# Kernel tuning notes

Hardware: AMD Instinct MI355X
Metric: run time of the kernel (lower is better)

## Reference

```python
import jax, jax.numpy as jnp
import numpy as np

M, U, H, C, EMB, HID = 4096, 8, 8, 64, 64, 128
N = M * U            # 32768 nodes
E = 131072           # edges
D = H * C            # 512 = heads * hidden_channels
NUM_LAYERS = 4
IN0 = 6              # 2 coords + mask + speed + cost + arrival
SCALE = np.float32(1.0 / np.sqrt(C))

def _lin(x, W, b):
    return x @ W + b

def _transformer_conv(x, src, dst, Wq, bq, Wk, bk, Wv, bv, Ws, bs):
    # PyG TransformerConv: x_j = x[src], x_i = x[dst]; softmax over edges per dst
    n = x.shape[0]
    q = _lin(x, Wq, bq).reshape(n, H, C)
    k = _lin(x, Wk, bk).reshape(n, H, C)
    v = _lin(x, Wv, bv).reshape(n, H, C)
    alpha = jnp.einsum('ehc,ehc->eh', q[dst], k[src]) * SCALE   # [E,H]
    amax = jax.ops.segment_max(alpha, dst, num_segments=n)       # [N,H]
    ex = jnp.exp(alpha - amax[dst])
    denom = jax.ops.segment_sum(ex, dst, num_segments=n)         # [N,H]
    agg = jax.ops.segment_sum(ex[:, :, None] * v[src], dst, num_segments=n)  # [N,H,C]
    out = agg / (denom[:, :, None] + 1e-16)
    return out.reshape(n, D) + _lin(x, Ws, bs)                   # concat heads + root skip

def _forward(mission_coords, uavs_info, speeds, cost_matrix, arrival_times,
             Wq0, bq0, Wk0, bk0, Wv0, bv0, Ws0, bs0,
             Wq, bq, Wk, bk, Wv, bv, Ws, bs,
             fc_W, fc_b, aW1, ab1, aW2, ab2, cW1, cb1, cW2, cb2,
             edge_index, batch, action_mask):
    mc = jnp.broadcast_to(mission_coords[:, None, :], (M, U, 2))
    mk = jnp.broadcast_to(action_mask[:, None, None].astype(jnp.float32), (M, U, 1))
    sp = jnp.broadcast_to(speeds[None, :, None], (M, U, 1))
    cm = cost_matrix.T[:, :, None]
    at = arrival_times.T[:, :, None]
    x = jnp.concatenate([mc, mk, sp, cm, at], axis=-1).reshape(N, IN0)
    src, dst = edge_index[0], edge_index[1]
    x = jax.nn.relu(_transformer_conv(x, src, dst, Wq0, bq0, Wk0, bk0, Wv0, bv0, Ws0, bs0))
    for l in range(NUM_LAYERS - 1):
        x = jax.nn.relu(_transformer_conv(x, src, dst, Wq[l], bq[l], Wk[l], bk[l], Wv[l], bv[l], Ws[l], bs[l]))
    new_batch = jnp.repeat(batch, U)                             # [N]
    sums = jax.ops.segment_sum(x, new_batch, num_segments=1)
    cnts = jax.ops.segment_sum(jnp.ones((N,), x.dtype), new_batch, num_segments=1)
    pooled = sums / cnts[:, None]                                # [1, D]
    emb = _lin(pooled, fc_W, fc_b)                               # [1, EMB]
    emb_exp = jnp.tile(emb, (U, 1))                              # [U, EMB]
    combined = jnp.concatenate([uavs_info, emb_exp, speeds[:, None]], axis=-1)  # [U, EMB+3]
    action_probs = jax.nn.softmax(_lin(jax.nn.relu(_lin(combined, aW1, ab1)), aW2, ab2), axis=-1)
    state_values = _lin(jax.nn.relu(_lin(combined, cW1, cb1)), cW2, cb2)
    return action_probs, state_values

def setup_inputs() -> dict:
    key = jax.random.key(0)
    ks = jax.random.split(key, 40)
    def nrm(i, shape, s=0.05):
        return jax.random.normal(ks[i], shape, jnp.float32) * s
    z = lambda *s: jnp.zeros(s, jnp.float32)
    L = NUM_LAYERS - 1
    inp = dict(
        mission_coords=jax.random.uniform(ks[0], (M, 2), jnp.float32),
        uavs_info=nrm(1, (U, 2), 1.0),
        speeds=jax.random.uniform(ks[2], (U,), jnp.float32) + 0.5,
        cost_matrix=jax.random.uniform(ks[3], (U, M), jnp.float32),
        arrival_times=jax.random.uniform(ks[4], (U, M), jnp.float32),
        edge_index=jax.random.randint(ks[5], (2, E), 0, N),
        batch=jnp.zeros((M,), jnp.int32),
        action_mask=jax.random.randint(ks[6], (M,), 0, 2),
        Wq0=nrm(7, (IN0, D)), bq0=z(D), Wk0=nrm(8, (IN0, D)), bk0=z(D),
        Wv0=nrm(9, (IN0, D)), bv0=z(D), Ws0=nrm(10, (IN0, D)), bs0=z(D),
        Wq=nrm(11, (L, D, D)), bq=z(L, D), Wk=nrm(12, (L, D, D)), bk=z(L, D),
        Wv=nrm(13, (L, D, D)), bv=z(L, D), Ws=nrm(14, (L, D, D)), bs=z(L, D),
        fc_W=nrm(15, (D, EMB)), fc_b=z(EMB),
        aW1=nrm(16, (EMB + 3, HID)), ab1=z(HID), aW2=nrm(17, (HID, M)), ab2=z(M),
        cW1=nrm(18, (EMB + 3, HID)), cb1=z(HID), cW2=nrm(19, (HID, 1)), cb2=z(1),
    )
    return inp

def reference(mission_coords, edge_index, batch, uavs_info, action_mask, speeds,
              cost_matrix, arrival_times,
              Wq0, bq0, Wk0, bk0, Wv0, bv0, Ws0, bs0,
              Wq, bq, Wk, bk, Wv, bv, Ws, bs,
              fc_W, fc_b, aW1, ab1, aW2, ab2, cW1, cb1, cW2, cb2):
    return _forward(mission_coords, uavs_info, speeds, cost_matrix, arrival_times,
                    Wq0, bq0, Wk0, bk0, Wv0, bv0, Ws0, bs0,
                    Wq, bq, Wk, bk, Wv, bv, Ws, bs,
                    fc_W, fc_b, aW1, ab1, aW2, ab2, cW1, cb1, cW2, cb2,
                    edge_index, batch, action_mask)
```

## Files before the change

kernel.cpp:

```cpp
#include <hip/hip_runtime.h>
#include <stdint.h>

typedef unsigned short u16;
typedef __attribute__((ext_vector_type(8))) unsigned short u16x8;
typedef __attribute__((ext_vector_type(8))) __bf16 bf16x8;
typedef __attribute__((ext_vector_type(4))) float f32x4;
typedef __attribute__((ext_vector_type(2))) float f32x2;

#define NNODES 32768
#define NEDGES 131072
#define DDIM 512
#define QK4 2048
#define MM 4096
#define UU 8

__device__ __forceinline__ u16 f2bf(float f) {
    unsigned u = __builtin_bit_cast(unsigned, f);
    u += 0x7FFFu + ((u >> 16) & 1u);
    return (u16)(u >> 16);
}
__device__ __forceinline__ float bf2f(u16 h) {
    return __builtin_bit_cast(float, (unsigned)h << 16);
}

__device__ __forceinline__ void enc8(const float* f, int* lo, int* hi) {
    int a = __builtin_amdgcn_cvt_pk_fp8_f32(f[0], f[1], 0, false);
    a = __builtin_amdgcn_cvt_pk_fp8_f32(f[2], f[3], a, true);
    int b = __builtin_amdgcn_cvt_pk_fp8_f32(f[4], f[5], 0, false);
    b = __builtin_amdgcn_cvt_pk_fp8_f32(f[6], f[7], b, true);
    *lo = a;
    *hi = b;
}

__device__ __forceinline__ void load_lds16(const void* g, void* l) {
    __builtin_amdgcn_global_load_lds((__attribute__((address_space(1))) unsigned int*)(void*)g,
                                     (__attribute__((address_space(3))) unsigned int*)l, 16, 0, 0);
}

__global__ void k_zero(unsigned int* p, int n) {
    int i = blockIdx.x * 256 + threadIdx.x;
    if (i < n) p[i] = 0u;
}

__global__ void k_build_x0(const float* __restrict__ mc, const int* __restrict__ mask,
                           const float* __restrict__ sp, const float* __restrict__ cm,
                           const float* __restrict__ at, float* __restrict__ x0) {
    int node = blockIdx.x * 256 + threadIdx.x;
    if (node >= NNODES) return;
    int m = node >> 3, u = node & 7;
    float* o = x0 + (size_t)node * 6;
    o[0] = mc[m * 2];
    o[1] = mc[m * 2 + 1];
    o[2] = (float)mask[m];
    o[3] = sp[u];
    o[4] = cm[u * MM + m];
    o[5] = at[u * MM + m];
}

__global__ void k_w0cat(const float* __restrict__ Wq0, const float* __restrict__ Wk0,
                        const float* __restrict__ Wv0, const float* __restrict__ Ws0,
                        float* __restrict__ W0cat) {
    int i = blockIdx.x * 256 + threadIdx.x;
    if (i >= 6 * QK4) return;
    int k = i / QK4, n = i % QK4;
    int t = n >> 9, nn = n & 511;
    const float* p = (t == 0) ? Wq0 : (t == 1) ? Wk0 : (t == 2) ? Wv0 : Ws0;
    W0cat[i] = p[k * DDIM + nn];
}

__global__ void k_bcat(const float* __restrict__ bq0, const float* __restrict__ bk0,
                       const float* __restrict__ bv0, const float* __restrict__ bs0,
                       const float* __restrict__ bq, const float* __restrict__ bk,
                       const float* __restrict__ bv, const float* __restrict__ bs,
                       float* __restrict__ b0cat, float* __restrict__ bcat) {
    int i = blockIdx.x * 256 + threadIdx.x;
    if (i >= 4 * QK4) return;
    int n = i & (QK4 - 1);
    int l = i >> 11;
    int t = n >> 9, nn = n & 511;
    if (l == 0) {
        const float* p = (t == 0) ? bq0 : (t == 1) ? bk0 : (t == 2) ? bv0 : bs0;
        b0cat[n] = p[nn];
    } else {
        const float* p = (t == 0) ? bq : (t == 1) ? bk : (t == 2) ? bv : bs;
        bcat[(size_t)(l - 1) * QK4 + n] = p[(l - 1) * DDIM + nn];
    }
}

__global__ void k_wt(const float* __restrict__ Wq, const float* __restrict__ Wk,
                     const float* __restrict__ Wv, const float* __restrict__ Ws,
                     u16* __restrict__ Wt) {
    __shared__ float tile[32][33];
    int q = blockIdx.z;
    int l = q >> 2, t = q & 3;
    const float* src = ((t == 0) ? Wq : (t == 1) ? Wk : (t == 2) ? Wv : Ws) + (size_t)l * DDIM * DDIM;
    int k0 = blockIdx.x * 32, n0 = blockIdx.y * 32;
    int tx = threadIdx.x, ty = threadIdx.y;
#pragma unroll
    for (int r = 0; r < 4; r++) tile[ty + 8 * r][tx] = src[(size_t)(k0 + ty + 8 * r) * DDIM + n0 + tx];
    __syncthreads();
    u16* dst = Wt + (size_t)l * QK4 * DDIM + (size_t)t * DDIM * DDIM;
#pragma unroll
    for (int r = 0; r < 4; r++) {
        int n = n0 + ty + 8 * r;
        dst[(size_t)n * DDIM + k0 + tx] = f2bf(tile[tx][ty + 8 * r]);
    }
}

__global__ void k_count(const int* __restrict__ dst, int* __restrict__ deg) {
    int e = blockIdx.x * 256 + threadIdx.x;
    if (e < NEDGES) atomicAdd(&deg[dst[e]], 1);
}

__global__ __launch_bounds__(1024) void k_scan(const int* __restrict__ deg, int* __restrict__ offs,
                                               int* __restrict__ cursor) {
    __shared__ int sums[1024];
    int t = threadIdx.x;
    int base = t * 32;
    int local[32];
    int s = 0;
#pragma unroll
    for (int i = 0; i < 32; i++) { local[i] = s; s += deg[base + i]; }
    sums[t] = s;
    __syncthreads();
    for (int d = 1; d < 1024; d <<= 1) {
        int v = (t >= d) ? sums[t - d] : 0;
        __syncthreads();
        sums[t] += v;
        __syncthreads();
    }
    int excl = (t == 0) ? 0 : sums[t - 1];
#pragma unroll
    for (int i = 0; i < 32; i++) {
        int o = excl + local[i];
        offs[base + i] = o;
        cursor[base + i] = o;
    }
    if (t == 1023) offs[NNODES] = sums[1023];
}

__global__ void k_scatter(const int* __restrict__ src, const int* __restrict__ dst,
                          int* __restrict__ cursor, int* __restrict__ ssrc) {
    int e = blockIdx.x * 256 + threadIdx.x;
    if (e < NEDGES) {
        int pos = atomicAdd(&cursor[dst[e]], 1);
        ssrc[pos] = src[e];
    }
}

__global__ __launch_bounds__(256) void k_gemm0(const float* __restrict__ x0, const float* __restrict__ W0cat,
                                               const float* __restrict__ b0cat, u16* __restrict__ QS,
                                               unsigned char* __restrict__ KV8) {
    int node = blockIdx.x;
    int t = threadIdx.x;
    float xv[6];
#pragma unroll
    for (int k = 0; k < 6; k++) xv[k] = x0[(size_t)node * 6 + k];
    int n0 = t * 8;
    float f[8];
#pragma unroll
    for (int j = 0; j < 8; j++) {
        int n = n0 + j;
        float s = b0cat[n];
#pragma unroll
        for (int k = 0; k < 6; k++) s += xv[k] * W0cat[k * QK4 + n];
        f[j] = s;
    }
    if (n0 < 512) {
        u16x8 o;
#pragma unroll
        for (int j = 0; j < 8; j++) o[j] = f2bf(f[j]);
        *(u16x8*)(QS + (size_t)node * 1024 + n0) = o;
    } else if (n0 < 1536) {
        int lo, hi;
        enc8(f, &lo, &hi);
        int kvcol = (n0 < 1024) ? (n0 - 512) : (n0 - 1024);
        int ofs = (n0 < 1024) ? 0 : 8;
        *(int2*)(KV8 + (size_t)node * 1024 + (size_t)(kvcol >> 3) * 16 + ofs) = make_int2(lo, hi);
    } else {
        u16x8 o;
#pragma unroll
        for (int j = 0; j < 8; j++) o[j] = f2bf(f[j]);
        *(u16x8*)(QS + (size_t)node * 1024 + 512 + (n0 - 1536)) = o;
    }
}

__global__ __launch_bounds__(256, 4) void k_gemm(const u16* __restrict__ X, const u16* __restrict__ Wt,
                                                 const float* __restrict__ bcat, u16* __restrict__ QS,
                                                 unsigned char* __restrict__ KV8) {
    __shared__ __align__(16) u16 smem[2 * 128 * 64];
    u16* As = smem;
    u16* Bs = smem + 128 * 64;
    const int tid = threadIdx.x;
    const int lane = tid & 63;
    const int w = tid >> 6;
    const int wm = w & 1, wn = w >> 1;
    const int bid = blockIdx.x;
    const int xcd = bid & 7;
    const int s = bid >> 3;
    const size_t arow0 = (size_t)(xcd * 32 + (s >> 4)) * 128;
    const size_t brow0 = (size_t)(s & 15) * 128;
    const int bt = (int)(brow0 >> 7);

    f32x4 acc[4][4];
#pragma unroll
    for (int i = 0; i < 4; i++)
#pragma unroll
        for (int j = 0; j < 4; j++) acc[i][j] = (f32x4){0.f, 0.f, 0.f, 0.f};

    const int la = lane & 7;
    const int quad = lane >> 4;
    const int lm = lane & 15;

    for (int kt = 0; kt < 8; ++kt) {
        const int k0 = kt * 64;
#pragma unroll
        for (int t = 0; t < 4; ++t) {
            int idx = (w * 4 + t) * 64 + lane;
            int m = idx >> 3;
            int c = la ^ (m & 7);
            const u16* ga = X + (arow0 + m) * DDIM + (k0 + c * 8);
            const u16* gb = Wt + (brow0 + m) * DDIM + (k0 + c * 8);
            load_lds16(ga, &As[(size_t)((w * 4 + t) * 64) * 8]);
            load_lds16(gb, &Bs[(size_t)((w * 4 + t) * 64) * 8]);
        }
        __syncthreads();
#pragma unroll
        for (int kk = 0; kk < 2; ++kk) {
            bf16x8 af[4], bfg[4];
            int c = kk * 4 + quad;
#pragma unroll
            for (int i = 0; i < 4; ++i) {
                int m = wm * 64 + i * 16 + lm;
                int slot = m * 8 + (c ^ (m & 7));
                af[i] = *(const bf16x8*)&As[(size_t)slot * 8];
            }
#pragma unroll
            for (int j = 0; j < 4; ++j) {
                int n = wn * 64 + j * 16 + lm;
                int slot = n * 8 + (c ^ (n & 7));
                bfg[j] = *(const bf16x8*)&Bs[(size_t)slot * 8];
            }
#pragma unroll
            for (int i = 0; i < 4; ++i)
#pragma unroll
                for (int j = 0; j < 4; ++j)
                    acc[i][j] = __builtin_amdgcn_mfma_f32_16x16x32_bf16(af[i], bfg[j], acc[i][j], 0, 0, 0);
        }
        __syncthreads();
    }

    float biasv[4];
#pragma unroll
    for (int j = 0; j < 4; ++j) biasv[j] = bcat[brow0 + wn * 64 + j * 16 + lm];

    u16* stg = smem;
    const int chunk = lane & 7;
    const int rrow = lane >> 3;
    const int colbase = (int)brow0 + wn * 64 + chunk * 8;
#pragma unroll
    for (int p = 0; p < 2; ++p) {
        __syncthreads();
#pragma unroll
        for (int ii = 0; ii < 2; ++ii) {
            int i = p * 2 + ii;
#pragma unroll
            for (int j = 0; j < 4; ++j) {
#pragma unroll
                for (int r = 0; r < 4; ++r) {
                    int lr = ii * 16 + quad * 4 + r;
                    int lc = j * 16 + lm;
                    stg[(size_t)(w * 32 + lr) * 72 + lc] = f2bf(acc[i][j][r] + biasv[j]);
                }
            }
        }
        __syncthreads();
#pragma unroll
        for (int it = 0; it < 4; ++it) {
            int row = it * 8 + rrow;
            u16x8 v = *(const u16x8*)&stg[(size_t)(w * 32 + row) * 72 + chunk * 8];
            size_t grow = arow0 + wm * 64 + p * 32 + row;
            if (bt < 4) {
                *(u16x8*)&QS[grow * 1024 + colbase] = v;
            } else if (bt < 12) {
                float f[8];
#pragma unroll
                for (int j = 0; j < 8; j++) f[j] = bf2f(v[j]);
                int lo, hi;
                enc8(f, &lo, &hi);
                int kvcol = (bt < 8) ? (colbase - 512) : (colbase - 1024);
                int ofs = (bt < 8) ? 0 : 8;
                *(int2*)(KV8 + grow * 1024 + (size_t)(kvcol >> 3) * 16 + ofs) = make_int2(lo, hi);
            } else {
                *(u16x8*)&QS[grow * 1024 + 512 + (colbase - 1536)] = v;
            }
        }
    }
}

__global__ __launch_bounds__(256) void k_attn(const u16* __restrict__ QS, const unsigned char* __restrict__ KV8,
                                              const int* __restrict__ offs, const int* __restrict__ ssrc,
                                              u16* __restrict__ Xout) {
    const int lane = threadIdx.x & 63;
    const int node = blockIdx.x * 4 + (threadIdx.x >> 6);
    const int c0 = lane * 8;
    const u16x8 qv = *(const u16x8*)(QS + (size_t)node * 1024 + c0);
    float qf[8];
#pragma unroll
    for (int j = 0; j < 8; j++) qf[j] = bf2f(qv[j]);
    float m = -INFINITY, l = 0.f;
    float acc[8];
#pragma unroll
    for (int j = 0; j < 8; j++) acc[j] = 0.f;
    const int e0 = offs[node], e1 = offs[node + 1];
    for (int e = e0; e < e1; ++e) {
        int s = ssrc[e];
        int4 kv = *(const int4*)(KV8 + (size_t)s * 1024 + (size_t)lane * 16);
        f32x2 k01 = __builtin_amdgcn_cvt_pk_f32_fp8(kv.x, false);
        f32x2 k23 = __builtin_amdgcn_cvt_pk_f32_fp8(kv.x, true);
        f32x2 k45 = __builtin_amdgcn_cvt_pk_f32_fp8(kv.y, false);
        f32x2 k67 = __builtin_amdgcn_cvt_pk_f32_fp8(kv.y, true);
        float d = qf[0] * k01[0] + qf[1] * k01[1] + qf[2] * k23[0] + qf[3] * k23[1] +
                  qf[4] * k45[0] + qf[5] * k45[1] + qf[6] * k67[0] + qf[7] * k67[1];
        d += __shfl_xor(d, 1, 64);
        d += __shfl_xor(d, 2, 64);
        d += __shfl_xor(d, 4, 64);
        float a = d * 0.125f;
        float nm = fmaxf(m, a);
        float corr = __expf(m - nm);
        float p = __expf(a - nm);
        l = l * corr + p;
        f32x2 v01 = __builtin_amdgcn_cvt_pk_f32_fp8(kv.z, false);
        f32x2 v23 = __builtin_amdgcn_cvt_pk_f32_fp8(kv.z, true);
        f32x2 v45 = __builtin_amdgcn_cvt_pk_f32_fp8(kv.w, false);
        f32x2 v67 = __builtin_amdgcn_cvt_pk_f32_fp8(kv.w, true);
        acc[0] = acc[0] * corr + p * v01[0];
        acc[1] = acc[1] * corr + p * v01[1];
        acc[2] = acc[2] * corr + p * v23[0];
        acc[3] = acc[3] * corr + p * v23[1];
        acc[4] = acc[4] * corr + p * v45[0];
        acc[5] = acc[5] * corr + p * v45[1];
        acc[6] = acc[6] * corr + p * v67[0];
        acc[7] = acc[7] * corr + p * v67[1];
        m = nm;
    }
    float inv = 1.0f / (l + 1e-16f);
    const u16x8 sv = *(const u16x8*)(QS + (size_t)node * 1024 + 512 + c0);
    u16x8 o;
#pragma unroll
    for (int j = 0; j < 8; j++) {
        float r = acc[j] * inv + bf2f(sv[j]);
        o[j] = f2bf(fmaxf(r, 0.f));
    }
    *(u16x8*)(Xout + (size_t)node * DDIM + c0) = o;
}

__global__ __launch_bounds__(256) void k_pool(const u16* __restrict__ X, float* __restrict__ pooled) {
    __shared__ float red[4][64][8];
    int t = threadIdx.x;
    int chunk = t & 63;
    int rofs = t >> 6;
    float s[8];
#pragma unroll
    for (int j = 0; j < 8; j++) s[j] = 0.f;
    int nd0 = blockIdx.x * 256;
    for (int nd = nd0 + rofs; nd < nd0 + 256; nd += 4) {
        u16x8 v = *(const u16x8*)&X[(size_t)nd * DDIM + chunk * 8];
#pragma unroll
        for (int j = 0; j < 8; j++) s[j] += bf2f(v[j]);
    }
#pragma unroll
    for (int j = 0; j < 8; j++) red[rofs][chunk][j] = s[j];
    __syncthreads();
    if (t < 64) {
#pragma unroll
        for (int j = 0; j < 8; j++) {
            float o = red[0][t][j] + red[1][t][j] + red[2][t][j] + red[3][t][j];
            atomicAdd(&pooled[t * 8 + j], o);
        }
    }
}

__global__ __launch_bounds__(1024) void k_heads(const float* __restrict__ pooled, const float* __restrict__ fcW,
                                                const float* __restrict__ fcb, const float* __restrict__ ui,
                                                const float* __restrict__ sp, const float* __restrict__ aW1,
                                                const float* __restrict__ ab1, const float* __restrict__ cW1,
                                                const float* __restrict__ cb1, const float* __restrict__ cW2,
                                                const float* __restrict__ cb2, float* __restrict__ hidden_a,
                                                float* __restrict__ out) {
    __shared__ float spool[512];
    __shared__ float semb[64];
    __shared__ float shc[8][128];
    int t = threadIdx.x;
    if (t < 512) spool[t] = pooled[t] * (1.0f / 32768.0f);
    __syncthreads();
    if (t < 64) {
        float s = fcb[t];
        for (int k = 0; k < 512; k++) s += spool[k] * fcW[k * 64 + t];
        semb[t] = s;
    }
    __syncthreads();
    int u = t >> 7, j = t & 127;
    float u0 = ui[u * 2], u1 = ui[u * 2 + 1], uspd = sp[u];
    float ha = ab1[j] + u0 * aW1[j] + u1 * aW1[128 + j] + uspd * aW1[66 * 128 + j];
    float hc = cb1[j] + u0 * cW1[j] + u1 * cW1[128 + j] + uspd * cW1[66 * 128 + j];
    for (int k = 0; k < 64; k++) {
        float e = semb[k];
        ha += e * aW1[(2 + k) * 128 + j];
        hc += e * cW1[(2 + k) * 128 + j];
    }
    ha = fmaxf(ha, 0.f);
    hc = fmaxf(hc, 0.f);
    hidden_a[u * 128 + j] = ha;
    shc[u][j] = hc;
    __syncthreads();
    if (t < 8) {
        float s = cb2[0];
        for (int k = 0; k < 128; k++) s += shc[t][k] * cW2[k];
        out[NNODES + t] = s;
    }
}

__global__ __launch_bounds__(1024) void k_actor(const float* __restrict__ hidden_a, const float* __restrict__ aW2,
                                                const float* __restrict__ ab2, float* __restrict__ out) {
    __shared__ float h[128];
    __shared__ float red[1024];
    int u = blockIdx.x, t = threadIdx.x;
    if (t < 128) h[t] = hidden_a[u * 128 + t];
    __syncthreads();
    float lg[4];
#pragma unroll
    for (int p = 0; p < 4; p++) {
        int mcol = t + p * 1024;
        float s = ab2[mcol];
        for (int k = 0; k < 128; k++) s += h[k] * aW2[(size_t)k * MM + mcol];
        lg[p] = s;
    }
    float mx = fmaxf(fmaxf(lg[0], lg[1]), fmaxf(lg[2], lg[3]));
    red[t] = mx;
    __syncthreads();
    for (int s2 = 512; s2 > 0; s2 >>= 1) {
        if (t < s2) red[t] = fmaxf(red[t], red[t + s2]);
        __syncthreads();
    }
    mx = red[0];
    __syncthreads();
    float e[4], sum = 0.f;
#pragma unroll
    for (int p = 0; p < 4; p++) {
        e[p] = __expf(lg[p] - mx);
        sum += e[p];
    }
    red[t] = sum;
    __syncthreads();
    for (int s2 = 512; s2 > 0; s2 >>= 1) {
        if (t < s2) red[t] += red[t + s2];
        __syncthreads();
    }
    float inv = 1.0f / red[0];
#pragma unroll
    for (int p = 0; p < 4; p++) out[(size_t)u * MM + t + p * 1024] = e[p] * inv;
}

extern "C" void kernel_launch(void* const* d_in, const int* in_sizes, int n_in,
                              void* d_out, int out_size, void* d_ws, size_t ws_size,
                              hipStream_t stream) {
    const float* mc   = (const float*)d_in[0];
    const float* ui   = (const float*)d_in[1];
    const float* sp   = (const float*)d_in[2];
    const float* cm   = (const float*)d_in[3];
    const float* at   = (const float*)d_in[4];
    const int*   eidx = (const int*)d_in[5];
    const int*   mask = (const int*)d_in[7];
    const float* Wq0 = (const float*)d_in[8];
    const float* bq0 = (const float*)d_in[9];
    const float* Wk0 = (const float*)d_in[10];
    const float* bk0 = (const float*)d_in[11];
    const float* Wv0 = (const float*)d_in[12];
    const float* bv0 = (const float*)d_in[13];
    const float* Ws0 = (const float*)d_in[14];
    const float* bs0 = (const float*)d_in[15];
    const float* Wq = (const float*)d_in[16];
    const float* bq = (const float*)d_in[17];
    const float* Wk = (const float*)d_in[18];
    const float* bk = (const float*)d_in[19];
    const float* Wv = (const float*)d_in[20];
    const float* bv = (const float*)d_in[21];
    const float* Ws = (const float*)d_in[22];
    const float* bs = (const float*)d_in[23];
    const float* fcW = (const float*)d_in[24];
    const float* fcb = (const float*)d_in[25];
    const float* aW1 = (const float*)d_in[26];
    const float* ab1 = (const float*)d_in[27];
    const float* aW2 = (const float*)d_in[28];
    const float* ab2 = (const float*)d_in[29];
    const float* cW1 = (const float*)d_in[30];
    const float* cb1 = (const float*)d_in[31];
    const float* cW2 = (const float*)d_in[32];
    const float* cb2 = (const float*)d_in[33];
    float* out = (float*)d_out;

    const int* esrc = eidx;
    const int* edst = eidx + NEDGES;

    char* ws = (char*)d_ws;
    size_t off = 0;
    auto alloc = [&](size_t bytes) -> void* {
        void* p = ws + off;
        off += (bytes + 255) & ~(size_t)255;
        return p;
    };
    u16*   QS    = (u16*)alloc((size_t)NNODES * 1024 * 2);
    unsigned char* KV8 = (unsigned char*)alloc((size_t)NNODES * 1024);
    u16*   X     = (u16*)alloc((size_t)NNODES * DDIM * 2);
    u16*   Wt    = (u16*)alloc((size_t)3 * QK4 * DDIM * 2);
    float* W0cat = (float*)alloc((size_t)6 * QK4 * 4);
    float* b0cat = (float*)alloc((size_t)QK4 * 4);
    float* bcat  = (float*)alloc((size_t)3 * QK4 * 4);
    float* x0    = (float*)alloc((size_t)NNODES * 6 * 4);
    int*   deg   = (int*)alloc((size_t)NNODES * 4);
    int*   offs  = (int*)alloc((size_t)(NNODES + 1) * 4);
    int*   cursor= (int*)alloc((size_t)NNODES * 4);
    int*   ssrc  = (int*)alloc((size_t)NEDGES * 4);
    float* pooled= (float*)alloc((size_t)512 * 4);
    float* hidden_a = (float*)alloc((size_t)UU * 128 * 4);
    (void)ws_size; (void)in_sizes; (void)n_in; (void)out_size;

    k_zero<<<(NNODES + 255) / 256, 256, 0, stream>>>((unsigned int*)deg, NNODES);
    k_zero<<<2, 256, 0, stream>>>((unsigned int*)pooled, 512);
    k_build_x0<<<NNODES / 256, 256, 0, stream>>>(mc, mask, sp, cm, at, x0);
    k_w0cat<<<(6 * QK4 + 255) / 256, 256, 0, stream>>>(Wq0, Wk0, Wv0, Ws0, W0cat);
    k_bcat<<<(4 * QK4 + 255) / 256, 256, 0, stream>>>(bq0, bk0, bv0, bs0, bq, bk, bv, bs, b0cat, bcat);
    {
        dim3 g(16, 16, 12), b(32, 8);
        k_wt<<<g, b, 0, stream>>>(Wq, Wk, Wv, Ws, Wt);
    }
    k_count<<<NEDGES / 256, 256, 0, stream>>>(edst, deg);
    k_scan<<<1, 1024, 0, stream>>>(deg, offs, cursor);
    k_scatter<<<NEDGES / 256, 256, 0, stream>>>(esrc, edst, cursor, ssrc);

    k_gemm0<<<NNODES, 256, 0, stream>>>(x0, W0cat, b0cat, QS, KV8);
    k_attn<<<NNODES / 4, 256, 0, stream>>>(QS, KV8, offs, ssrc, X);

    for (int l = 0; l < 3; ++l) {
        k_gemm<<<4096, 256, 0, stream>>>(X, Wt + (size_t)l * QK4 * DDIM, bcat + (size_t)l * QK4, QS, KV8);
        k_attn<<<NNODES / 4, 256, 0, stream>>>(QS, KV8, offs, ssrc, X);
    }

    k_pool<<<128, 256, 0, stream>>>(X, pooled);
    k_heads<<<1, 1024, 0, stream>>>(pooled, fcW, fcb, ui, sp, aW1, ab1, cW1, cb1, cW2, cb2, hidden_a, out);
    k_actor<<<UU, 1024, 0, stream>>>(hidden_a, aW2, ab2, out);
}
```

Before: 660.7 us.

## Pack Q/K/V/skip into one interleaved row, store Q in fp8, prefetch edges

Merges the separate QS (bf16 Q and skip) and KV8 (fp8 K/V) buffers into a single 2560-byte row per node. Q is now stored as fp8 instead of bf16, and the attention loop software-prefetches the next neighbour's K/V row. It also fuses five small setup kernels into one prep launch and raises the GEMM launch-bounds occupancy hint from 4 to 5. The aim is less memory traffic and latency in the gather-heavy attention and fewer launches, at the cost of extra fp8 rounding error on Q and possible register spills in the GEMM.

```diff
diff --git a/kernel.cpp b/kernel.cpp
--- a/kernel.cpp
+++ b/kernel.cpp
@@ -1,7 +1,9 @@
 #include <hip/hip_runtime.h>
 #include <stdint.h>
 
+typedef unsigned char u8;
 typedef unsigned short u16;
+typedef unsigned long long u64;
 typedef __attribute__((ext_vector_type(8))) unsigned short u16x8;
 typedef __attribute__((ext_vector_type(8))) __bf16 bf16x8;
 typedef __attribute__((ext_vector_type(4))) float f32x4;
@@ -13,6 +15,7 @@
 #define QK4 2048
 #define MM 4096
 #define UU 8
+#define ROWB 2560
 
 __device__ __forceinline__ u16 f2bf(float f) {
     unsigned u = __builtin_bit_cast(unsigned, f);
@@ -22,7 +25,6 @@
 __device__ __forceinline__ float bf2f(u16 h) {
     return __builtin_bit_cast(float, (unsigned)h << 16);
 }
-
 __device__ __forceinline__ void enc8(const float* f, int* lo, int* hi) {
     int a = __builtin_amdgcn_cvt_pk_fp8_f32(f[0], f[1], 0, false);
     a = __builtin_amdgcn_cvt_pk_fp8_f32(f[2], f[3], a, true);
@@ -31,59 +33,65 @@
     *lo = a;
     *hi = b;
 }
+__device__ __forceinline__ void dec8(int lo, int hi, float* f) {
+    f32x2 a = __builtin_amdgcn_cvt_pk_f32_fp8(lo, false);
+    f32x2 b = __builtin_amdgcn_cvt_pk_f32_fp8(lo, true);
+    f32x2 c = __builtin_amdgcn_cvt_pk_f32_fp8(hi, false);
+    f32x2 d = __builtin_amdgcn_cvt_pk_f32_fp8(hi, true);
+    f[0] = a[0]; f[1] = a[1]; f[2] = b[0]; f[3] = b[1];
+    f[4] = c[0]; f[5] = c[1]; f[6] = d[0]; f[7] = d[1];
+}
 
 __device__ __forceinline__ void load_lds16(const void* g, void* l) {
     __builtin_amdgcn_global_load_lds((__attribute__((address_space(1))) unsigned int*)(void*)g,
                                      (__attribute__((address_space(3))) unsigned int*)l, 16, 0, 0);
 }
 
-__global__ void k_zero(unsigned int* p, int n) {
-    int i = blockIdx.x * 256 + threadIdx.x;
-    if (i < n) p[i] = 0u;
-}
-
-__global__ void k_build_x0(const float* __restrict__ mc, const int* __restrict__ mask,
-                           const float* __restrict__ sp, const float* __restrict__ cm,
-                           const float* __restrict__ at, float* __restrict__ x0) {
-    int node = blockIdx.x * 256 + threadIdx.x;
-    if (node >= NNODES) return;
-    int m = node >> 3, u = node & 7;
-    float* o = x0 + (size_t)node * 6;
-    o[0] = mc[m * 2];
-    o[1] = mc[m * 2 + 1];
-    o[2] = (float)mask[m];
-    o[3] = sp[u];
-    o[4] = cm[u * MM + m];
-    o[5] = at[u * MM + m];
-}
-
-__global__ void k_w0cat(const float* __restrict__ Wq0, const float* __restrict__ Wk0,
-                        const float* __restrict__ Wv0, const float* __restrict__ Ws0,
-                        float* __restrict__ W0cat) {
-    int i = blockIdx.x * 256 + threadIdx.x;
-    if (i >= 6 * QK4) return;
-    int k = i / QK4, n = i % QK4;
-    int t = n >> 9, nn = n & 511;
-    const float* p = (t == 0) ? Wq0 : (t == 1) ? Wk0 : (t == 2) ? Wv0 : Ws0;
-    W0cat[i] = p[k * DDIM + nn];
-}
-
-__global__ void k_bcat(const float* __restrict__ bq0, const float* __restrict__ bk0,
+__global__ void k_prep(const float* __restrict__ mc, const int* __restrict__ mask,
+                       const float* __restrict__ sp, const float* __restrict__ cm,
+                       const float* __restrict__ at, float* __restrict__ x0,
+                       const float* __restrict__ Wq0, const float* __restrict__ Wk0,
+                       const float* __restrict__ Wv0, const float* __restrict__ Ws0,
+                       float* __restrict__ W0cat,
+                       const float* __restrict__ bq0, const float* __restrict__ bk0,
                        const float* __restrict__ bv0, const float* __restrict__ bs0,
                        const float* __restrict__ bq, const float* __restrict__ bk,
                        const float* __restrict__ bv, const float* __restrict__ bs,
-                       float* __restrict__ b0cat, float* __restrict__ bcat) {
-    int i = blockIdx.x * 256 + threadIdx.x;
-    if (i >= 4 * QK4) return;
-    int n = i & (QK4 - 1);
-    int l = i >> 11;
-    int t = n >> 9, nn = n & 511;
-    if (l == 0) {
-        const float* p = (t == 0) ? bq0 : (t == 1) ? bk0 : (t == 2) ? bv0 : bs0;
-        b0cat[n] = p[nn];
+                       float* __restrict__ b0cat, float* __restrict__ bcat,
+                       int* __restrict__ deg, float* __restrict__ pooled) {
+    int b = blockIdx.x;
+    int t = threadIdx.x;
+    if (b < 128) {
+        int node = b * 256 + t;
+        deg[node] = 0;
+        int m = node >> 3, u = node & 7;
+        float* o = x0 + (size_t)node * 6;
+        o[0] = mc[m * 2];
+        o[1] = mc[m * 2 + 1];
+        o[2] = (float)mask[m];
+        o[3] = sp[u];
+        o[4] = cm[u * MM + m];
+        o[5] = at[u * MM + m];
+    } else if (b < 176) {
+        int i = (b - 128) * 256 + t;
+        int k = i / QK4, n = i % QK4;
+        int ty = n >> 9, nn = n & 511;
+        const float* p = (ty == 0) ? Wq0 : (ty == 1) ? Wk0 : (ty == 2) ? Wv0 : Ws0;
+        W0cat[i] = p[k * DDIM + nn];
+    } else if (b < 208) {
+        int i = (b - 176) * 256 + t;
+        int n = i & (QK4 - 1);
+        int l = i >> 11;
+        int ty = n >> 9, nn = n & 511;
+        if (l == 0) {
+            const float* p = (ty == 0) ? bq0 : (ty == 1) ? bk0 : (ty == 2) ? bv0 : bs0;
+            b0cat[n] = p[nn];
+        } else {
+            const float* p = (ty == 0) ? bq : (ty == 1) ? bk : (ty == 2) ? bv : bs;
+            bcat[(size_t)(l - 1) * QK4 + n] = p[(l - 1) * DDIM + nn];
+        }
     } else {
-        const float* p = (t == 0) ? bq : (t == 1) ? bk : (t == 2) ? bv : bs;
-        bcat[(size_t)(l - 1) * QK4 + n] = p[(l - 1) * DDIM + nn];
+        pooled[(b - 208) * 256 + t] = 0.f;
     }
 }
 
@@ -148,9 +156,15 @@
     }
 }
 
+__device__ __forceinline__ size_t route_off(int col) {
+    if (col < 512) return (size_t)col;
+    if (col < 1024) return 512 + (size_t)((col - 512) >> 3) * 16;
+    if (col < 1536) return 512 + (size_t)((col - 1024) >> 3) * 16 + 8;
+    return 1536 + (size_t)(col - 1536) * 2;
+}
+
 __global__ __launch_bounds__(256) void k_gemm0(const float* __restrict__ x0, const float* __restrict__ W0cat,
-                                               const float* __restrict__ b0cat, u16* __restrict__ QS,
-                                               unsigned char* __restrict__ KV8) {
+                                               const float* __restrict__ b0cat, u8* __restrict__ QKVS) {
     int node = blockIdx.x;
     int t = threadIdx.x;
     float xv[6];
@@ -166,28 +180,21 @@
         for (int k = 0; k < 6; k++) s += xv[k] * W0cat[k * QK4 + n];
         f[j] = s;
     }
-    if (n0 < 512) {
-        u16x8 o;
-#pragma unroll
-        for (int j = 0; j < 8; j++) o[j] = f2bf(f[j]);
-        *(u16x8*)(QS + (size_t)node * 1024 + n0) = o;
-    } else if (n0 < 1536) {
+    size_t goff = route_off(n0);
+    if (n0 < 1536) {
         int lo, hi;
         enc8(f, &lo, &hi);
-        int kvcol = (n0 < 1024) ? (n0 - 512) : (n0 - 1024);
-        int ofs = (n0 < 1024) ? 0 : 8;
-        *(int2*)(KV8 + (size_t)node * 1024 + (size_t)(kvcol >> 3) * 16 + ofs) = make_int2(lo, hi);
+        *(int2*)(QKVS + (size_t)node * ROWB + goff) = make_int2(lo, hi);
     } else {
         u16x8 o;
 #pragma unroll
         for (int j = 0; j < 8; j++) o[j] = f2bf(f[j]);
-        *(u16x8*)(QS + (size_t)node * 1024 + 512 + (n0 - 1536)) = o;
-    }
-}
-
-__global__ __launch_bounds__(256, 4) void k_gemm(const u16* __restrict__ X, const u16* __restrict__ Wt,
-                                                 const float* __restrict__ bcat, u16* __restrict__ QS,
-                                                 unsigned char* __restrict__ KV8) {
+        *(u16x8*)(QKVS + (size_t)node * ROWB + goff) = o;
+    }
+}
+
+__global__ __launch_bounds__(256, 5) void k_gemm(const u16* __restrict__ X, const u16* __restrict__ Wt,
+                                                 const float* __restrict__ bcat, u8* __restrict__ QKVS) {
     __shared__ __align__(16) u16 smem[2 * 128 * 64];
     u16* As = smem;
     u16* Bs = smem + 128 * 64;
@@ -258,6 +265,7 @@
     const int chunk = lane & 7;
     const int rrow = lane >> 3;
     const int colbase = (int)brow0 + wn * 64 + chunk * 8;
+    const size_t goff = route_off(colbase);
 #pragma unroll
     for (int p = 0; p < 2; ++p) {
         __syncthreads();
@@ -280,42 +288,37 @@
             int row = it * 8 + rrow;
             u16x8 v = *(const u16x8*)&stg[(size_t)(w * 32 + row) * 72 + chunk * 8];
             size_t grow = arow0 + wm * 64 + p * 32 + row;
-            if (bt < 4) {
-                *(u16x8*)&QS[grow * 1024 + colbase] = v;
-            } else if (bt < 12) {
+            if (bt < 12) {
                 float f[8];
 #pragma unroll
                 for (int j = 0; j < 8; j++) f[j] = bf2f(v[j]);
                 int lo, hi;
                 enc8(f, &lo, &hi);
-                int kvcol = (bt < 8) ? (colbase - 512) : (colbase - 1024);
-                int ofs = (bt < 8) ? 0 : 8;
-                *(int2*)(KV8 + grow * 1024 + (size_t)(kvcol >> 3) * 16 + ofs) = make_int2(lo, hi);
+                *(int2*)(QKVS + grow * ROWB + goff) = make_int2(lo, hi);
             } else {
-                *(u16x8*)&QS[grow * 1024 + 512 + (colbase - 1536)] = v;
+                *(u16x8*)(QKVS + grow * ROWB + goff) = v;
             }
         }
     }
 }
 
-__global__ __launch_bounds__(256) void k_attn(const u16* __restrict__ QS, const unsigned char* __restrict__ KV8,
-                                              const int* __restrict__ offs, const int* __restrict__ ssrc,
-                                              u16* __restrict__ Xout) {
+__global__ __launch_bounds__(256) void k_attn(const u8* __restrict__ QKVS, const int* __restrict__ offs,
+                                              const int* __restrict__ ssrc, u16* __restrict__ Xout) {
     const int lane = threadIdx.x & 63;
     const int node = blockIdx.x * 4 + (threadIdx.x >> 6);
-    const int c0 = lane * 8;
-    const u16x8 qv = *(const u16x8*)(QS + (size_t)node * 1024 + c0);
+    const u64 q8 = *(const u64*)(QKVS + (size_t)node * ROWB + (size_t)lane * 8);
     float qf[8];
-#pragma unroll
-    for (int j = 0; j < 8; j++) qf[j] = bf2f(qv[j]);
+    dec8((int)(q8 & 0xFFFFFFFFull), (int)(q8 >> 32), qf);
     float m = -INFINITY, l = 0.f;
     float acc[8];
 #pragma unroll
     for (int j = 0; j < 8; j++) acc[j] = 0.f;
     const int e0 = offs[node], e1 = offs[node + 1];
+    int4 kvn;
+    if (e0 < e1) kvn = *(const int4*)(QKVS + (size_t)ssrc[e0] * ROWB + 512 + (size_t)lane * 16);
     for (int e = e0; e < e1; ++e) {
-        int s = ssrc[e];
-        int4 kv = *(const int4*)(KV8 + (size_t)s * 1024 + (size_t)lane * 16);
+        int4 kv = kvn;
+        if (e + 1 < e1) kvn = *(const int4*)(QKVS + (size_t)ssrc[e + 1] * ROWB + 512 + (size_t)lane * 16);
         f32x2 k01 = __builtin_amdgcn_cvt_pk_f32_fp8(kv.x, false);
         f32x2 k23 = __builtin_amdgcn_cvt_pk_f32_fp8(kv.x, true);
         f32x2 k45 = __builtin_amdgcn_cvt_pk_f32_fp8(kv.y, false);
@@ -345,14 +348,14 @@
         m = nm;
     }
     float inv = 1.0f / (l + 1e-16f);
-    const u16x8 sv = *(const u16x8*)(QS + (size_t)node * 1024 + 512 + c0);
+    const u16x8 sv = *(const u16x8*)(QKVS + (size_t)node * ROWB + 1536 + (size_t)lane * 16);
     u16x8 o;
 #pragma unroll
     for (int j = 0; j < 8; j++) {
         float r = acc[j] * inv + bf2f(sv[j]);
         o[j] = f2bf(fmaxf(r, 0.f));
     }
-    *(u16x8*)(Xout + (size_t)node * DDIM + c0) = o;
+    *(u16x8*)(Xout + (size_t)node * DDIM + (size_t)lane * 8) = o;
 }
 
 __global__ __launch_bounds__(256) void k_pool(const u16* __restrict__ X, float* __restrict__ pooled) {
@@ -510,8 +513,7 @@
         off += (bytes + 255) & ~(size_t)255;
         return p;
     };
-    u16*   QS    = (u16*)alloc((size_t)NNODES * 1024 * 2);
-    unsigned char* KV8 = (unsigned char*)alloc((size_t)NNODES * 1024);
+    u8*    QKVS  = (u8*)alloc((size_t)NNODES * ROWB);
     u16*   X     = (u16*)alloc((size_t)NNODES * DDIM * 2);
     u16*   Wt    = (u16*)alloc((size_t)3 * QK4 * DDIM * 2);
     float* W0cat = (float*)alloc((size_t)6 * QK4 * 4);
@@ -526,11 +528,8 @@
     float* hidden_a = (float*)alloc((size_t)UU * 128 * 4);
     (void)ws_size; (void)in_sizes; (void)n_in; (void)out_size;
 
-    k_zero<<<(NNODES + 255) / 256, 256, 0, stream>>>((unsigned int*)deg, NNODES);
-    k_zero<<<2, 256, 0, stream>>>((unsigned int*)pooled, 512);
-    k_build_x0<<<NNODES / 256, 256, 0, stream>>>(mc, mask, sp, cm, at, x0);
-    k_w0cat<<<(6 * QK4 + 255) / 256, 256, 0, stream>>>(Wq0, Wk0, Wv0, Ws0, W0cat);
-    k_bcat<<<(4 * QK4 + 255) / 256, 256, 0, stream>>>(bq0, bk0, bv0, bs0, bq, bk, bv, bs, b0cat, bcat);
+    k_prep<<<210, 256, 0, stream>>>(mc, mask, sp, cm, at, x0, Wq0, Wk0, Wv0, Ws0, W0cat,
+                                    bq0, bk0, bv0, bs0, bq, bk, bv, bs, b0cat, bcat, deg, pooled);
     {
         dim3 g(16, 16, 12), b(32, 8);
         k_wt<<<g, b, 0, stream>>>(Wq, Wk, Wv, Ws, Wt);
@@ -539,12 +538,12 @@
     k_scan<<<1, 1024, 0, stream>>>(deg, offs, cursor);
     k_scatter<<<NEDGES / 256, 256, 0, stream>>>(esrc, edst, cursor, ssrc);
 
-    k_gemm0<<<NNODES, 256, 0, stream>>>(x0, W0cat, b0cat, QS, KV8);
-    k_attn<<<NNODES / 4, 256, 0, stream>>>(QS, KV8, offs, ssrc, X);
+    k_gemm0<<<NNODES, 256, 0, stream>>>(x0, W0cat, b0cat, QKVS);
+    k_attn<<<NNODES / 4, 256, 0, stream>>>(QKVS, offs, ssrc, X);
 
     for (int l = 0; l < 3; ++l) {
-        k_gemm<<<4096, 256, 0, stream>>>(X, Wt + (size_t)l * QK4 * DDIM, bcat + (size_t)l * QK4, QS, KV8);
-        k_attn<<<NNODES / 4, 256, 0, stream>>>(QS, KV8, offs, ssrc, X);
+        k_gemm<<<4096, 256, 0, stream>>>(X, Wt + (size_t)l * QK4 * DDIM, bcat + (size_t)l * QK4, QKVS);
+        k_attn<<<NNODES / 4, 256, 0, stream>>>(QKVS, offs, ssrc, X);
     }
 
     k_pool<<<128, 256, 0, stream>>>(X, pooled);
```

Measured after the change: 872.0 us. +32.0%, slower.
